# Optimization experiments

Measured on AMD Instinct MI355X. Metric: run time of the kernel, lower is better.

## Reference

```python
import jax, jax.numpy as jnp
import numpy as np

HEADS, DIM = 4, 32
HID = HEADS * DIM
K = 8

def gelu(x):
    return jax.nn.gelu(x, approximate=False)

def seg_softmax(logits, seg, n):
    m = jax.ops.segment_max(logits, seg, num_segments=n)
    e = jnp.exp(logits - m[seg])
    s = jax.ops.segment_sum(e, seg, num_segments=n)
    return e / (s[seg] + 1e-16)

def layer_norm(x, g, b, eps=1e-5):
    mu = x.mean(-1, keepdims=True)
    var = ((x - mu) ** 2).mean(-1, keepdims=True)
    return (x - mu) * jax.lax.rsqrt(var + eps) * g + b

def hgt_layer(xa, xb, edges, Wkqv, bkqv, Wout, bout, skip, arel, mrel, prel):
    # One HGTConv: per-type kqv, per-edge-type DxD relation transforms,
    # global scatter-softmax over destination nodes, per-type output + gated skip.
    Na, Nb = xa.shape[0], xb.shape[0]
    N = Na + Nb
    def kqv(x, W, b):
        o = x @ W + b
        k, q, v = jnp.split(o, 3, -1)
        r = lambda t: t.reshape(-1, HEADS, DIM)
        return r(k), r(q), r(v)
    ka, qa, va = kqv(xa, Wkqv[0], bkqv[0])
    kb, qb, vb = kqv(xb, Wkqv[1], bkqv[1])
    # edge types: a->a, a->b, b->a  (dst offset places dst in global node space)
    specs = [(ka, va, qa, 0), (ka, va, qb, Na), (kb, vb, qa, 0)]
    alphas, msgs, dsts = [], [], []
    inv_sqrt_d = np.float32(1.0 / np.sqrt(DIM))
    for et, ((k_s, v_s, q_d, off), ei) in enumerate(zip(specs, edges)):
        src, dst = ei[0], ei[1]
        kt = jnp.einsum('nhd,hde->nhe', k_s, arel[et])  # per-head relation transform
        vt = jnp.einsum('nhd,hde->nhe', v_s, mrel[et])
        a = (q_d[dst] * kt[src]).sum(-1) * prel[et] * inv_sqrt_d  # [E,H]
        alphas.append(a); msgs.append(vt[src]); dsts.append(dst + off)
    alpha = jnp.concatenate(alphas, 0)
    msg = jnp.concatenate(msgs, 0)
    dst = jnp.concatenate(dsts, 0)
    w = seg_softmax(alpha, dst, N)
    agg = jax.ops.segment_sum(w[..., None] * msg, dst, num_segments=N).reshape(N, HID)
    def finish(o, x, t):
        g = gelu(o) @ Wout[t] + bout[t]
        s = jax.nn.sigmoid(skip[t])
        return s * g + (1.0 - s) * x
    return finish(agg[:Na], xa, 0), finish(agg[Na:], xb, 1)

def _forward(x_a, x_b, Wkqv, bkqv, Wout, bout, skip, arel, mrel, prel, ln_g, ln_b,
             Wgat, att_src, att_dst, bgat, W1, b1, W2, b2, W3, b3,
             ei_aa, ei_ab, ei_ba):
    edges = (ei_aa, ei_ab, ei_ba)
    ha, hb = x_a, x_b
    for L in range(3):
        ha, hb = hgt_layer(ha, hb, edges, Wkqv[L], bkqv[L], Wout[L], bout[L],
                           skip[L], arel[L], mrel[L], prel[L])
        if L == 0:  # norm after conv1 only (dropout is identity at inference)
            ha = layer_norm(ha, ln_g[0], ln_b[0])
            hb = layer_norm(hb, ln_g[1], ln_b[1])
        ha, hb = gelu(ha), gelu(hb)
    # to_homogeneous: concat node types in metadata order, offset edge indices
    Na = ha.shape[0]
    h = jnp.concatenate([ha, hb], 0)
    N = h.shape[0]
    loop = jnp.arange(N, dtype=ei_aa.dtype)
    src = jnp.concatenate([ei_aa[0], ei_ab[0], ei_ba[0] + Na, loop])  # GAT adds self loops
    dst = jnp.concatenate([ei_aa[1], ei_ab[1] + Na, ei_ba[1], loop])
    # SAGPooling scorer: GATConv(hid, 1, heads=1)
    x1 = h @ Wgat  # [N,1]
    e = jax.nn.leaky_relu((x1[src] * att_src + x1[dst] * att_dst).sum(-1), 0.2)
    w = seg_softmax(e, dst, N)
    score = (jax.ops.segment_sum(w[:, None] * x1[src], dst, num_segments=N) + bgat).squeeze(-1)
    vals, perm = jax.lax.top_k(score, K)
    hp = (h[perm] * jnp.tanh(vals)[:, None]).reshape(-1)  # [K*HID]
    v = gelu(hp @ W1 + b1)
    v = gelu(v @ W2 + b2)
    v = gelu(v @ W3 + b3)
    return jnp.nan_to_num(v)

def setup_inputs() -> dict:
    key = jax.random.key(0)
    ks = jax.random.split(key, 16)
    Na = Nb = 20000
    E = 150000
    g = lambda i, shape, s: jax.random.normal(ks[i], shape, jnp.float32) * s
    return {
        "x_a": g(0, (Na, 128), 1.0),
        "x_b": g(1, (Nb, 128), 1.0),
        "ei_aa": jax.random.randint(ks[2], (2, E), 0, Na, jnp.int32),
        "ei_ab": jax.random.randint(ks[3], (2, E), 0, Na, jnp.int32),
        "ei_ba": jax.random.randint(ks[4], (2, E), 0, Na, jnp.int32),
        "Wkqv": g(5, (3, 2, 128, 384), 0.05),
        "bkqv": jnp.zeros((3, 2, 384), jnp.float32),
        "Wout": g(6, (3, 2, 128, 128), 0.05),
        "bout": jnp.zeros((3, 2, 128), jnp.float32),
        "skip": jnp.ones((3, 2), jnp.float32),
        "arel": g(7, (3, 3, HEADS, DIM, DIM), 0.1),
        "mrel": g(8, (3, 3, HEADS, DIM, DIM), 0.1),
        "prel": jnp.ones((3, 3, HEADS), jnp.float32),
        "ln_g": jnp.ones((2, 128), jnp.float32),
        "ln_b": jnp.zeros((2, 128), jnp.float32),
        "Wgat": g(9, (128, 1), 0.1),
        "att_src": g(10, (1,), 1.0),
        "att_dst": g(11, (1,), 1.0),
        "bgat": jnp.zeros((1,), jnp.float32),
        "W1": g(12, (K * HID, 128), 0.03),
        "b1": jnp.zeros((128,), jnp.float32),
        "W2": g(13, (128, 64), 0.1),
        "b2": jnp.zeros((64,), jnp.float32),
        "W3": g(14, (64, 16), 0.1),
        "b3": jnp.zeros((16,), jnp.float32),
    }

def reference(x_a, x_b, ei_aa, ei_ab, ei_ba, Wkqv, bkqv, Wout, bout, skip,
              arel, mrel, prel, ln_g, ln_b, Wgat, att_src, att_dst, bgat,
              W1, b1, W2, b2, W3, b3):
    return _forward(x_a, x_b, Wkqv, bkqv, Wout, bout, skip, arel, mrel, prel,
                    ln_g, ln_b, Wgat, att_src, att_dst, bgat,
                    W1, b1, W2, b2, W3, b3, ei_aa, ei_ab, ei_ba)
```

## Files before the change

### kernel.cpp

```cpp
#include <hip/hip_runtime.h>
#include <math.h>

#define HID 128

__device__ __forceinline__ float gelu_f(float x){
  return 0.5f*x*(1.0f+erff(x*0.70710678118654752440f));
}

__global__ void mkw(const float* __restrict__ Wkqv, const float* __restrict__ bkqv,
                    const float* __restrict__ arel, const float* __restrict__ mrel,
                    const float* __restrict__ prel,
                    float* __restrict__ Wc, float* __restrict__ bc) {
  int L = blockIdx.x >> 10;
  int j = blockIdx.x & 1023;
  int t = threadIdx.x;
  int type = (j < 640) ? 0 : 1;
  int jj = (j < 640) ? j : j - 640;
  const float* W    = Wkqv + ((size_t)L*2 + type)*49152;
  const float* bsrc = bkqv + ((size_t)L*2 + type)*384;
  int stride = type ? 384 : 640;
  float* Wdst = Wc + (size_t)L*(640+384)*128 + (type ? (size_t)640*128 : 0);
  float* bdst = bc + (size_t)L*1024 + (type ? 640 : 0);
  float val, bval;
  if (jj < 128) {
    val  = W[(size_t)t*384 + 128 + jj];
    bval = bsrc[128 + jj];
  } else {
    int u = jj - 128;
    int et = type ? 2 : (u >> 8);
    int r = u & 255;
    int h = r >> 6, wofs = r & 63;
    const float* rel; int coloff; float scl;
    if (wofs < 32) {
      rel = arel + ((size_t)L*3 + et)*4096 + (size_t)h*32*32 + wofs;
      coloff = h*32;
      scl = prel[((size_t)L*3 + et)*4 + h] * 0.17677669529663688f * 1.4426950408889634f;
    } else {
      rel = mrel + ((size_t)L*3 + et)*4096 + (size_t)h*32*32 + (wofs - 32);
      coloff = 256 + h*32;
      scl = 1.0f;
    }
    float a = 0.f, bb = 0.f;
    for (int d = 0; d < 32; d++) {
      float rv = rel[(size_t)d*32];
      a  += W[(size_t)t*384 + coloff + d] * rv;
      bb += bsrc[coloff + d] * rv;
    }
    val = a * scl; bval = bb * scl;
  }
  Wdst[(size_t)t*stride + jj] = val;
  if (t == 0) bdst[jj] = bval;
}

__global__ __launch_bounds__(256, 2)
void gemm_tile(const float* __restrict__ x, const float* __restrict__ Wc,
               const float* __restrict__ bc,
               float* __restrict__ qbuf, float* __restrict__ ktv,
               int nrows, int OUT, int qoff, int slot0, int slot1) {
  __shared__ float xs[32][132];
  __shared__ float ws[32][128];
  int tid = threadIdx.x;
  int r0 = blockIdx.x * 128;
  int ct = blockIdx.y;
  int ty = tid >> 4, tx = tid & 15;
  float acc[8][8] = {};
  for (int kc = 0; kc < 128; kc += 32) {
    __syncthreads();
#pragma unroll
    for (int it = 0; it < 4; it++) {
      int idx = it*256 + tid;
      int r = idx >> 3;
      int k4 = (idx & 7) << 2;
      int row = r0 + r;
      float4 v = (row < nrows) ? *(const float4*)(x + (size_t)row*128 + kc + k4)
                               : make_float4(0.f, 0.f, 0.f, 0.f);
      xs[k4+0][r] = v.x; xs[k4+1][r] = v.y; xs[k4+2][r] = v.z; xs[k4+3][r] = v.w;
    }
#pragma unroll
    for (int it = 0; it < 4; it++) {
      int idx = it*256 + tid;
      int k = idx >> 5;
      int c4 = (idx & 31) << 2;
      *(float4*)&ws[k][c4] = *(const float4*)(Wc + (size_t)(kc + k)*OUT + ct*128 + c4);
    }
    __syncthreads();
#pragma unroll
    for (int k = 0; k < 32; k++) {
      float4 a0 = *(const float4*)&xs[k][ty*4];
      float4 a1 = *(const float4*)&xs[k][64 + ty*4];
      float4 b0 = *(const float4*)&ws[k][tx*4];
      float4 b1 = *(const float4*)&ws[k][64 + tx*4];
      float av[8] = {a0.x,a0.y,a0.z,a0.w,a1.x,a1.y,a1.z,a1.w};
      float bv[8] = {b0.x,b0.y,b0.z,b0.w,b1.x,b1.y,b1.z,b1.w};
#pragma unroll
      for (int i = 0; i < 8; i++)
#pragma unroll
        for (int j = 0; j < 8; j++)
          acc[i][j] += av[i]*bv[j];
    }
  }
  bool isq = (ct == 0);
  int sbase = 0, cofs = 0;
  if (!isq) {
    if (ct <= 2) { sbase = slot0; cofs = (ct-1)*128; }
    else         { sbase = slot1; cofs = (ct-3)*128; }
  }
#pragma unroll
  for (int i = 0; i < 8; i++) {
    int r = (i < 4) ? (ty*4 + i) : (64 + ty*4 + i - 4);
    int row = r0 + r;
    if (row >= nrows) continue;
#pragma unroll
    for (int half = 0; half < 2; half++) {
      int c0 = half*64 + tx*4;
      float4 v;
      v.x = acc[i][half*4+0] + bc[ct*128 + c0 + 0];
      v.y = acc[i][half*4+1] + bc[ct*128 + c0 + 1];
      v.z = acc[i][half*4+2] + bc[ct*128 + c0 + 2];
      v.w = acc[i][half*4+3] + bc[ct*128 + c0 + 3];
      if (isq) *(float4*)(qbuf + (size_t)(qoff + row)*128 + c0) = v;
      else     *(float4*)(ktv + (size_t)(sbase + row)*256 + cofs + c0) = v;
    }
  }
}

__global__ __launch_bounds__(256, 2)
void finish_tile(const float* __restrict__ agg,
                 const float* __restrict__ xa, const float* __restrict__ xb,
                 float* __restrict__ ha, float* __restrict__ hb,
                 const float* __restrict__ WoL, const float* __restrict__ boL,
                 const float* __restrict__ skipL, int do_gelu, int Na, int Nb) {
  __shared__ float xs[32][132];
  __shared__ float ws[32][128];
  int nba = (Na + 127) >> 7;
  const float *xsrc, *Wo, *bo; float* h; float sgraw; int nrows, r0, aggoff;
  if ((int)blockIdx.x < nba) {
    xsrc = xa; h = ha; Wo = WoL; bo = boL; sgraw = skipL[0];
    nrows = Na; r0 = blockIdx.x*128; aggoff = 0;
  } else {
    xsrc = xb; h = hb; Wo = WoL + 16384; bo = boL + 128; sgraw = skipL[1];
    nrows = Nb; r0 = ((int)blockIdx.x - nba)*128; aggoff = Na;
  }
  int tid = threadIdx.x;
  int ty = tid >> 4, tx = tid & 15;
  float acc[8][8] = {};
  for (int kc = 0; kc < 128; kc += 32) {
    __syncthreads();
#pragma unroll
    for (int it = 0; it < 4; it++) {
      int idx = it*256 + tid;
      int r = idx >> 3;
      int k4 = (idx & 7) << 2;
      int row = r0 + r;
      float4 v = (row < nrows)
        ? *(const float4*)(agg + (size_t)(aggoff + row)*128 + kc + k4)
        : make_float4(0.f, 0.f, 0.f, 0.f);
      xs[k4+0][r] = gelu_f(v.x); xs[k4+1][r] = gelu_f(v.y);
      xs[k4+2][r] = gelu_f(v.z); xs[k4+3][r] = gelu_f(v.w);
    }
#pragma unroll
    for (int it = 0; it < 4; it++) {
      int idx = it*256 + tid;
      int k = idx >> 5;
      int c4 = (idx & 31) << 2;
      *(float4*)&ws[k][c4] = *(const float4*)(Wo + (size_t)(kc + k)*128 + c4);
    }
    __syncthreads();
#pragma unroll
    for (int k = 0; k < 32; k++) {
      float4 a0 = *(const float4*)&xs[k][ty*4];
      float4 a1 = *(const float4*)&xs[k][64 + ty*4];
      float4 b0 = *(const float4*)&ws[k][tx*4];
      float4 b1 = *(const float4*)&ws[k][64 + tx*4];
      float av[8] = {a0.x,a0.y,a0.z,a0.w,a1.x,a1.y,a1.z,a1.w};
      float bv[8] = {b0.x,b0.y,b0.z,b0.w,b1.x,b1.y,b1.z,b1.w};
#pragma unroll
      for (int i = 0; i < 8; i++)
#pragma unroll
        for (int j = 0; j < 8; j++)
          acc[i][j] += av[i]*bv[j];
    }
  }
  float sg = 1.f/(1.f + expf(-sgraw));
#pragma unroll
  for (int i = 0; i < 8; i++) {
    int r = (i < 4) ? (ty*4 + i) : (64 + ty*4 + i - 4);
    int row = r0 + r;
    if (row >= nrows) continue;
#pragma unroll
    for (int half = 0; half < 2; half++) {
      int c0 = half*64 + tx*4;
      float4 xv = *(const float4*)(xsrc + (size_t)row*128 + c0);
      float4 v;
      v.x = sg*(acc[i][half*4+0] + bo[c0+0]) + (1.f - sg)*xv.x;
      v.y = sg*(acc[i][half*4+1] + bo[c0+1]) + (1.f - sg)*xv.y;
      v.z = sg*(acc[i][half*4+2] + bo[c0+2]) + (1.f - sg)*xv.z;
      v.w = sg*(acc[i][half*4+3] + bo[c0+3]) + (1.f - sg)*xv.w;
      if (do_gelu) { v.x = gelu_f(v.x); v.y = gelu_f(v.y); v.z = gelu_f(v.z); v.w = gelu_f(v.w); }
      *(float4*)(h + (size_t)row*128 + c0) = v;
    }
  }
}

__global__ void hist_init(int* __restrict__ hist, int N) {
  int i = blockIdx.x*blockDim.x + threadIdx.x;
  if (i < N) hist[i] = 0;
}
__global__ void hist_count_all(const int* __restrict__ aa, const int* __restrict__ ab,
                               const int* __restrict__ ba,
                               int Eaa, int Eab, int Eba, int Na, int* __restrict__ hist) {
  int i = blockIdx.x*blockDim.x + threadIdx.x;
  int tot = Eaa + Eab + Eba;
  if (i >= tot) return;
  int dst;
  if (i < Eaa)            dst = aa[Eaa + i];
  else if (i < Eaa + Eab) dst = ab[Eab + (i - Eaa)] + Na;
  else                    dst = ba[Eba + (i - Eaa - Eab)];
  atomicAdd(hist + dst, 1);
}
__global__ void scan_excl(const int* __restrict__ hist, int* __restrict__ roff, int N) {
  __shared__ int part[1024];
  int t = threadIdx.x;
  int chunk = (N + 1023) / 1024;
  int b = t*chunk, e = b + chunk; if (e > N) e = N; if (b > N) b = N;
  int sum = 0;
  for (int i = b; i < e; i++) sum += hist[i];
  part[t] = sum;
  __syncthreads();
  for (int o = 1; o < 1024; o <<= 1) {
    int v = (t >= o) ? part[t - o] : 0;
    __syncthreads();
    part[t] += v;
    __syncthreads();
  }
  int run = (t == 0) ? 0 : part[t - 1];
  for (int i = b; i < e; i++) { roff[i] = run; run += hist[i]; }
  if (t == 1023) roff[N] = run;
}
__global__ void fill_all(const int* __restrict__ aa, const int* __restrict__ ab,
                         const int* __restrict__ ba,
                         int Eaa, int Eab, int Eba, int Na,
                         int* __restrict__ cursor, int* __restrict__ epack) {
  int i = blockIdx.x*blockDim.x + threadIdx.x;
  int tot = Eaa + Eab + Eba;
  if (i >= tot) return;
  int dst, slot;
  if (i < Eaa)            { dst = aa[Eaa + i];                slot = aa[i]; }
  else if (i < Eaa + Eab) { int j = i - Eaa;       dst = ab[Eab + j] + Na; slot = ab[j] + Na; }
  else                    { int j = i - Eaa - Eab; dst = ba[Eba + j];      slot = ba[j] + 2*Na; }
  int pos = atomicAdd(cursor + dst, 1);
  epack[pos] = slot;
}

__global__ void seg_attn(const float* __restrict__ qbuf,
                         const float* __restrict__ ktv,
                         const int* __restrict__ roff, const int* __restrict__ epack,
                         float* __restrict__ agg, int Na, int N) {
  int wid = (blockIdx.x*blockDim.x + threadIdx.x) >> 6;
  int lane = threadIdx.x & 63;
  if (wid >= N) return;
  int h = lane >> 4;
  int d0 = (lane & 15) * 2;
  float2 q = *(const float2*)(qbuf + (size_t)wid*128 + h*32 + d0);
  int beg = roff[wid], end = roff[wid + 1];
  float m = -INFINITY, s = 0.f, a0 = 0.f, a1 = 0.f;
  if (beg < end) {
    const float* kp = ktv + (size_t)epack[beg]*256 + h*64 + d0;
    float2 kv = *(const float2*)kp;
    float2 vv = *(const float2*)(kp + 32);
    for (int i = beg; i < end; i++) {
      float2 ck = kv, cv = vv;
      if (i + 1 < end) {
        const float* kpn = ktv + (size_t)epack[i+1]*256 + h*64 + d0;
        kv = *(const float2*)kpn;
        vv = *(const float2*)(kpn + 32);
      }
      float sc = q.x*ck.x + q.y*ck.y;
      sc += __shfl_xor(sc, 1, 64);
      sc += __shfl_xor(sc, 2, 64);
      sc += __shfl_xor(sc, 4, 64);
      sc += __shfl_xor(sc, 8, 64);
      float nm = fmaxf(m, sc);
      float scale = exp2f(m - nm);
      float e = exp2f(sc - nm);
      s  = s*scale  + e;
      a0 = a0*scale + e*cv.x;
      a1 = a1*scale + e*cv.y;
      m = nm;
    }
  }
  float inv = 1.f / (s + 1e-16f);
  float2 o2; o2.x = a0*inv; o2.y = a1*inv;
  *(float2*)(agg + (size_t)wid*128 + h*32 + d0) = o2;
}

__global__ void ln_gelu2(float* __restrict__ h, const float* __restrict__ g,
                         const float* __restrict__ b, int Na, int N) {
  int idx = blockIdx.x*blockDim.x + threadIdx.x;
  int row = idx >> 6, lane = idx & 63;
  if (row >= N) return;
  int po = (row < Na) ? 0 : 128;
  float x0 = h[(size_t)row*128 + lane];
  float x1 = h[(size_t)row*128 + 64 + lane];
  float sum = x0 + x1;
#pragma unroll
  for (int o = 32; o; o >>= 1) sum += __shfl_xor(sum, o, 64);
  float mu = sum * (1.f/128.f);
  float d0 = x0 - mu, d1 = x1 - mu;
  float vs = d0*d0 + d1*d1;
#pragma unroll
  for (int o = 32; o; o >>= 1) vs += __shfl_xor(vs, o, 64);
  float inv = 1.f / sqrtf(vs*(1.f/128.f) + 1e-5f);
  h[(size_t)row*128 + lane]      = gelu_f(d0*inv*g[po + lane] + b[po + lane]);
  h[(size_t)row*128 + 64 + lane] = gelu_f(d1*inv*g[po + 64 + lane] + b[po + 64 + lane]);
}

__global__ void gat_x1(const float* __restrict__ h, const float* __restrict__ Wg,
                       float* __restrict__ x1, int N) {
  int idx = blockIdx.x*blockDim.x + threadIdx.x;
  int row = idx >> 6, lane = idx & 63;
  if (row >= N) return;
  float a = h[(size_t)row*128 + lane]*Wg[lane] + h[(size_t)row*128 + 64 + lane]*Wg[64 + lane];
#pragma unroll
  for (int o = 32; o; o >>= 1) a += __shfl_xor(a, o, 64);
  if (lane == 0) x1[row] = a;
}

__global__ void gat_all(const float* __restrict__ x1, const int* __restrict__ roff,
                        const int* __restrict__ epack,
                        const float* __restrict__ asrc, const float* __restrict__ adst,
                        int Na, int N, float* __restrict__ score) {
  int n = blockIdx.x*blockDim.x + threadIdx.x;
  if (n >= N) return;
  float xd = x1[n];
  float as_ = asrc[0], ad = adst[0];
  float e0 = xd*as_ + xd*ad;
  e0 = (e0 > 0.f) ? e0 : 0.2f*e0;
  float m = e0, s = 1.f, acc = xd;
  int beg = roff[n], end = roff[n + 1];
  for (int i = beg; i < end; i++) {
    int slot = epack[i];
    int sg = (slot < Na) ? slot : slot - Na;
    float xs = x1[sg];
    float e = xs*as_ + xd*ad;
    e = (e > 0.f) ? e : 0.2f*e;
    float nm = fmaxf(m, e);
    float sc = __expf(m - nm), ee = __expf(e - nm);
    s = s*sc + ee;  acc = acc*sc + ee*xs;  m = nm;
  }
  score[n] = acc / (s + 1e-16f);
}

__global__ void topk_stage1(const float* __restrict__ score, const float* __restrict__ bgat,
                            int N, float* __restrict__ cvals, int* __restrict__ cidx) {
  __shared__ float bv[256];
  __shared__ int   bi[256];
  int t = threadIdx.x;
  int chunk = (N + gridDim.x - 1) / gridDim.x;
  int i = blockIdx.x * chunk + t;
  float bg = bgat[0];
  bool valid = (t < chunk && i < N);
  float myv = valid ? score[i] + bg : -INFINITY;
  int   myi = valid ? i : 0x7FFFFFFF;
  for (int k = 0; k < 8; k++) {
    bv[t] = myv; bi[t] = myi;
    __syncthreads();
    for (int o = 128; o; o >>= 1) {
      if (t < o) {
        if (bv[t+o] > bv[t] || (bv[t+o] == bv[t] && bi[t+o] < bi[t])) { bv[t]=bv[t+o]; bi[t]=bi[t+o]; }
      }
      __syncthreads();
    }
    if (t == 0) { cvals[blockIdx.x*8 + k] = bv[0]; cidx[blockIdx.x*8 + k] = bi[0]; }
    if (myi == bi[0]) myv = -INFINITY;
    __syncthreads();
  }
}

__global__ void topk_stage2(const float* __restrict__ cvals, const int* __restrict__ cidx,
                            int C, float* __restrict__ vals, int* __restrict__ perm) {
  __shared__ float bv[256];
  __shared__ int   bi[256];
  __shared__ int   seli[8];
  int t = threadIdx.x;
  for (int k = 0; k < 8; k++) {
    float best = -INFINITY; int besti = 0x7FFFFFFF;
    for (int i = t; i < C; i += 256) {
      int id = cidx[i];
      bool taken = false;
      for (int j = 0; j < k; j++) if (seli[j] == id) taken = true;
      if (taken) continue;
      float v = cvals[i];
      if (v > best || (v == best && id < besti)) { best = v; besti = id; }
    }
    bv[t] = best; bi[t] = besti;
    __syncthreads();
    for (int o = 128; o; o >>= 1) {
      if (t < o) {
        if (bv[t+o] > bv[t] || (bv[t+o] == bv[t] && bi[t+o] < bi[t])) { bv[t]=bv[t+o]; bi[t]=bi[t+o]; }
      }
      __syncthreads();
    }
    if (t == 0) { seli[k] = bi[0]; vals[k] = bv[0]; perm[k] = bi[0]; }
    __syncthreads();
  }
}

__global__ void mlp_final(const float* __restrict__ h, const float* __restrict__ vals,
                          const int* __restrict__ perm,
                          const float* __restrict__ W1, const float* __restrict__ b1,
                          const float* __restrict__ W2, const float* __restrict__ b2,
                          const float* __restrict__ W3, const float* __restrict__ b3,
                          float* __restrict__ out) {
  __shared__ float hp[1024], v1[128], v2[64];
  int t = threadIdx.x;
  for (int i = t; i < 1024; i += 256) {
    int r = i >> 7, d = i & 127;
    hp[i] = h[(size_t)perm[r]*128 + d] * tanhf(vals[r]);
  }
  __syncthreads();
  if (t < 128) {
    float a = 0.f;
    for (int k = 0; k < 1024; k++) a += hp[k]*W1[(size_t)k*128 + t];
    v1[t] = gelu_f(a + b1[t]);
  }
  __syncthreads();
  if (t < 64) {
    float a = 0.f;
    for (int k = 0; k < 128; k++) a += v1[k]*W2[(size_t)k*64 + t];
    v2[t] = gelu_f(a + b2[t]);
  }
  __syncthreads();
  if (t < 16) {
    float a = 0.f;
    for (int k = 0; k < 64; k++) a += v2[k]*W3[(size_t)k*16 + t];
    float r = gelu_f(a + b3[t]);
    if (isnan(r)) r = 0.f;
    else if (isinf(r)) r = (r > 0.f) ? 3.4028234663852886e38f : -3.4028234663852886e38f;
    out[t] = r;
  }
}

extern "C" void kernel_launch(void* const* d_in, const int* in_sizes, int n_in,
                              void* d_out, int out_size, void* d_ws, size_t ws_size,
                              hipStream_t stream) {
  const float* x_a  = (const float*)d_in[0];
  const float* x_b  = (const float*)d_in[1];
  const int* ei_aa  = (const int*)d_in[2];
  const int* ei_ab  = (const int*)d_in[3];
  const int* ei_ba  = (const int*)d_in[4];
  const float* Wkqv = (const float*)d_in[5];
  const float* bkqv = (const float*)d_in[6];
  const float* Wout = (const float*)d_in[7];
  const float* bout = (const float*)d_in[8];
  const float* skip = (const float*)d_in[9];
  const float* arel = (const float*)d_in[10];
  const float* mrel = (const float*)d_in[11];
  const float* prel = (const float*)d_in[12];
  const float* ln_g = (const float*)d_in[13];
  const float* ln_b = (const float*)d_in[14];
  const float* Wgat = (const float*)d_in[15];
  const float* att_src = (const float*)d_in[16];
  const float* att_dst = (const float*)d_in[17];
  const float* bgat = (const float*)d_in[18];
  const float* W1 = (const float*)d_in[19];
  const float* b1 = (const float*)d_in[20];
  const float* W2 = (const float*)d_in[21];
  const float* b2 = (const float*)d_in[22];
  const float* W3 = (const float*)d_in[23];
  const float* b3 = (const float*)d_in[24];

  int Na = in_sizes[0]/128, Nb = in_sizes[1]/128, N = Na + Nb;
  int Eaa = in_sizes[2]/2, Eab = in_sizes[3]/2, Eba = in_sizes[4]/2;
  int Etot = Eaa + Eab + Eba;

  float* w = (float*)d_ws;
  size_t off = 0;
  auto alloc = [&](size_t n) { float* p = w + off; off += n; return p; };
  float* hbuf  = alloc((size_t)N*128);
  float* qbuf  = alloc((size_t)N*128);
  float* ktvA  = alloc((size_t)(2*Na + Nb)*256);
  float* agg   = alloc((size_t)N*128);
  float* Wc    = alloc((size_t)3*1024*128);
  float* bc    = alloc((size_t)3*1024);
  float* x1buf = alloc((size_t)N);
  float* score = alloc((size_t)N);
  float* valsb = alloc(8);
  int*   permb = (int*)alloc(8);
  float* cvals = alloc(2048);
  int*   cidx  = (int*)alloc(2048);
  int*   hist  = (int*)alloc((size_t)N);
  int*   roff  = (int*)alloc((size_t)N + 1);
  int*   cursor= (int*)alloc((size_t)N);
  int*   epack = (int*)alloc((size_t)Etot);

  float* h_a = hbuf;
  float* h_b = hbuf + (size_t)Na*128;

  mkw<<<dim3(3*1024),dim3(128),0,stream>>>(Wkqv, bkqv, arel, mrel, prel, Wc, bc);

  hist_init<<<dim3((N+255)/256),dim3(256),0,stream>>>(hist, N);
  hist_count_all<<<dim3((Etot+255)/256),dim3(256),0,stream>>>(ei_aa, ei_ab, ei_ba, Eaa, Eab, Eba, Na, hist);
  scan_excl<<<dim3(1),dim3(1024),0,stream>>>(hist, roff, N);
  hipMemcpyAsync(cursor, roff, (size_t)N*sizeof(int), hipMemcpyDeviceToDevice, stream);
  fill_all<<<dim3((Etot+255)/256),dim3(256),0,stream>>>(ei_aa, ei_ab, ei_ba, Eaa, Eab, Eba, Na, cursor, epack);

  int nba = (Na + 127)/128, nbb = (Nb + 127)/128;

  for (int L = 0; L < 3; L++) {
    const float* xa_in = (L == 0) ? x_a : h_a;
    const float* xb_in = (L == 0) ? x_b : h_b;
    const float* WcA = Wc + (size_t)L*1024*128;
    const float* WcB = WcA + (size_t)640*128;
    const float* bcA = bc + (size_t)L*1024;
    const float* bcB = bcA + 640;
    gemm_tile<<<dim3(nba, 5),dim3(256),0,stream>>>(xa_in, WcA, bcA, qbuf, ktvA, Na, 640, 0,  0,    Na);
    gemm_tile<<<dim3(nbb, 3),dim3(256),0,stream>>>(xb_in, WcB, bcB, qbuf, ktvA, Nb, 384, Na, 2*Na, 2*Na);
    seg_attn<<<dim3((N+3)/4),dim3(256),0,stream>>>(qbuf, ktvA, roff, epack, agg, Na, N);
    int do_gelu = (L == 0) ? 0 : 1;
    finish_tile<<<dim3(nba + nbb),dim3(256),0,stream>>>(agg, xa_in, xb_in, h_a, h_b,
                                                        Wout + (size_t)L*2*16384,
                                                        bout + (size_t)L*2*128,
                                                        skip + L*2, do_gelu, Na, Nb);
    if (L == 0) {
      ln_gelu2<<<dim3((N+3)/4),dim3(256),0,stream>>>(hbuf, ln_g, ln_b, Na, N);
    }
  }

  gat_x1<<<dim3((N+3)/4),dim3(256),0,stream>>>(hbuf, Wgat, x1buf, N);
  gat_all<<<dim3((N+255)/256),dim3(256),0,stream>>>(x1buf, roff, epack, att_src, att_dst, Na, N, score);
  int tk_blocks = (N + 255)/256;
  topk_stage1<<<dim3(tk_blocks),dim3(256),0,stream>>>(score, bgat, N, cvals, cidx);
  topk_stage2<<<dim3(1),dim3(256),0,stream>>>(cvals, cidx, tk_blocks*8, valsb, permb);
  mlp_final<<<dim3(1),dim3(256),0,stream>>>(hbuf, valsb, permb, W1, b1, W2, b2, W3, b3, (float*)d_out);
}
```

Before: 918.4 us.

## Split seg_attn wavefront into four edge-parallel groups with online-softmax merge

Each 64-lane wavefront now handles four incoming edges of a destination node at once. Every group of 16 lanes covers all four heads with 8 dims per lane and wide float4 loads, in place of walking the edges one at a time with 2 dims per lane. Each group keeps its own running max, sum and accumulator, and these are merged with cross-lane shuffles at the end. This is meant to shorten the serial edge loop and raise memory-level parallelism for gathered K/V rows, at the cost of more registers and a merge step.

```diff
diff --git a/kernel.cpp b/kernel.cpp
--- a/kernel.cpp
+++ b/kernel.cpp
@@ -259,39 +259,71 @@
   int wid = (blockIdx.x*blockDim.x + threadIdx.x) >> 6;
   int lane = threadIdx.x & 63;
   if (wid >= N) return;
-  int h = lane >> 4;
-  int d0 = (lane & 15) * 2;
-  float2 q = *(const float2*)(qbuf + (size_t)wid*128 + h*32 + d0);
+  int quarter = lane >> 4;
+  int u = lane & 15;
+  int h = u >> 2;
+  int d0 = (u & 3) * 8;
+  const float* qp = qbuf + (size_t)wid*128 + h*32 + d0;
+  float4 qa = *(const float4*)qp;
+  float4 qb = *(const float4*)(qp + 4);
   int beg = roff[wid], end = roff[wid + 1];
-  float m = -INFINITY, s = 0.f, a0 = 0.f, a1 = 0.f;
-  if (beg < end) {
-    const float* kp = ktv + (size_t)epack[beg]*256 + h*64 + d0;
-    float2 kv = *(const float2*)kp;
-    float2 vv = *(const float2*)(kp + 32);
-    for (int i = beg; i < end; i++) {
-      float2 ck = kv, cv = vv;
-      if (i + 1 < end) {
-        const float* kpn = ktv + (size_t)epack[i+1]*256 + h*64 + d0;
-        kv = *(const float2*)kpn;
-        vv = *(const float2*)(kpn + 32);
-      }
-      float sc = q.x*ck.x + q.y*ck.y;
-      sc += __shfl_xor(sc, 1, 64);
-      sc += __shfl_xor(sc, 2, 64);
-      sc += __shfl_xor(sc, 4, 64);
-      sc += __shfl_xor(sc, 8, 64);
-      float nm = fmaxf(m, sc);
-      float scale = exp2f(m - nm);
-      float e = exp2f(sc - nm);
-      s  = s*scale  + e;
-      a0 = a0*scale + e*cv.x;
-      a1 = a1*scale + e*cv.y;
-      m = nm;
-    }
-  }
-  float inv = 1.f / (s + 1e-16f);
-  float2 o2; o2.x = a0*inv; o2.y = a1*inv;
-  *(float2*)(agg + (size_t)wid*128 + h*32 + d0) = o2;
+  float m = -1e30f, s = 0.f;
+  float4 aA = make_float4(0.f,0.f,0.f,0.f), aB = make_float4(0.f,0.f,0.f,0.f);
+  int i = beg + quarter;
+  float4 ka, kb, va, vb;
+  if (i < end) {
+    const float* kp = ktv + (size_t)epack[i]*256 + h*64 + d0;
+    ka = *(const float4*)kp;      kb = *(const float4*)(kp + 4);
+    va = *(const float4*)(kp+32); vb = *(const float4*)(kp + 36);
+  }
+  for (; i < end; i += 4) {
+    float4 cka = ka, ckb = kb, cva = va, cvb = vb;
+    int nx = i + 4;
+    if (nx < end) {
+      const float* kp = ktv + (size_t)epack[nx]*256 + h*64 + d0;
+      ka = *(const float4*)kp;      kb = *(const float4*)(kp + 4);
+      va = *(const float4*)(kp+32); vb = *(const float4*)(kp + 36);
+    }
+    float sc = qa.x*cka.x + qa.y*cka.y + qa.z*cka.z + qa.w*cka.w
+             + qb.x*ckb.x + qb.y*ckb.y + qb.z*ckb.z + qb.w*ckb.w;
+    sc += __shfl_xor(sc, 1, 64);
+    sc += __shfl_xor(sc, 2, 64);
+    float nm = fmaxf(m, sc);
+    float scale = exp2f(m - nm);
+    float e = exp2f(sc - nm);
+    s = s*scale + e;
+    aA.x = aA.x*scale + e*cva.x; aA.y = aA.y*scale + e*cva.y;
+    aA.z = aA.z*scale + e*cva.z; aA.w = aA.w*scale + e*cva.w;
+    aB.x = aB.x*scale + e*cvb.x; aB.y = aB.y*scale + e*cvb.y;
+    aB.z = aB.z*scale + e*cvb.z; aB.w = aB.w*scale + e*cvb.w;
+    m = nm;
+  }
+#pragma unroll
+  for (int off = 16; off <= 32; off <<= 1) {
+    float mo = __shfl_xor(m, off, 64);
+    float so = __shfl_xor(s, off, 64);
+    float A0 = __shfl_xor(aA.x, off, 64), A1 = __shfl_xor(aA.y, off, 64);
+    float A2 = __shfl_xor(aA.z, off, 64), A3 = __shfl_xor(aA.w, off, 64);
+    float B0 = __shfl_xor(aB.x, off, 64), B1 = __shfl_xor(aB.y, off, 64);
+    float B2 = __shfl_xor(aB.z, off, 64), B3 = __shfl_xor(aB.w, off, 64);
+    float nm = fmaxf(m, mo);
+    float c1 = exp2f(m - nm), c2 = exp2f(mo - nm);
+    s = s*c1 + so*c2;
+    aA.x = aA.x*c1 + A0*c2; aA.y = aA.y*c1 + A1*c2;
+    aA.z = aA.z*c1 + A2*c2; aA.w = aA.w*c1 + A3*c2;
+    aB.x = aB.x*c1 + B0*c2; aB.y = aB.y*c1 + B1*c2;
+    aB.z = aB.z*c1 + B2*c2; aB.w = aB.w*c1 + B3*c2;
+    m = nm;
+  }
+  if (quarter == 0) {
+    float inv = 1.f / (s + 1e-16f);
+    float4 o1, o2;
+    o1.x = aA.x*inv; o1.y = aA.y*inv; o1.z = aA.z*inv; o1.w = aA.w*inv;
+    o2.x = aB.x*inv; o2.y = aB.y*inv; o2.z = aB.z*inv; o2.w = aB.w*inv;
+    float* op = agg + (size_t)wid*128 + h*32 + d0;
+    *(float4*)op = o1;
+    *(float4*)(op + 4) = o2;
+  }
 }
 
 __global__ void ln_gelu2(float* __restrict__ h, const float* __restrict__ g,
```

Measured after the change: 890.8 us. 1.03x faster.
